# Optimization experiments

Measured on AMD Instinct MI355X. Metric: run time of the kernel, lower is better.

Reference implementation:

```python
import jax, jax.numpy as jnp
import numpy as np

N_NODES = 100000

def gcn_conv(x, row, col, w, W, b, n):
    # PyG GCNConv with edge weights: add self-loops, symmetric normalization.
    loop = jnp.arange(n)
    r = jnp.concatenate([row, loop])
    c = jnp.concatenate([col, loop])
    ew = jnp.concatenate([w, jnp.ones((n,), dtype=x.dtype)])
    deg = jax.ops.segment_sum(ew, c, num_segments=n)          # [N]
    dinv = jnp.where(deg > 0, jax.lax.rsqrt(deg), 0.0)
    norm = dinv[r] * ew * dinv[c]                              # [E+N]
    h = x @ W                                                  # [N, C]
    msg = norm[:, None] * h[r]                                 # [E+N, C]
    out = jax.ops.segment_sum(msg, c, num_segments=n)          # [N, C]
    return out + b

def setup_inputs() -> dict:
    key = jax.random.key(0)
    ks = jax.random.split(key, 9)
    n, F, H, O = N_NODES, 128, 128, 64  # H = 2*out_channels
    E = 1600000
    x = jax.random.normal(ks[0], (n, F), dtype=jnp.float32)
    edge_index = jax.random.randint(ks[1], (2, E), 0, n, dtype=jnp.int64)
    edge_attr = jax.random.uniform(ks[2], (E,), dtype=jnp.float32)
    s = 1.0 / np.sqrt(F)
    W1 = jax.random.uniform(ks[3], (F, H), jnp.float32, -s, s)
    b1 = jnp.zeros((H,), jnp.float32)
    s2 = 1.0 / np.sqrt(H)
    Wmu = jax.random.uniform(ks[4], (H, O), jnp.float32, -s2, s2)
    bmu = jnp.zeros((O,), jnp.float32)
    Wls = jax.random.uniform(ks[5], (H, O), jnp.float32, -s2, s2)
    bls = jnp.zeros((O,), jnp.float32)
    return {"x": x, "edge_index": edge_index, "edge_attr": edge_attr,
            "W1": W1, "b1": b1, "Wmu": Wmu, "bmu": bmu, "Wls": Wls, "bls": bls}

def reference(x, edge_index, edge_attr, W1, b1, Wmu, bmu, Wls, bls):
    n = x.shape[0]
    row, col = edge_index[0], edge_index[1]
    h = jax.nn.relu(gcn_conv(x, row, col, edge_attr, W1, b1, n))
    mu = gcn_conv(h, row, col, edge_attr, Wmu, bmu, n)
    logstd = gcn_conv(h, row, col, edge_attr, Wls, bls, n)
    return (mu, logstd)
```

## Files before the change

kernel.cpp:

```cpp
#include <hip/hip_runtime.h>
#include <math.h>


#define NBLK 1024

typedef __attribute__((ext_vector_type(8))) short bf16x8;
typedef __attribute__((ext_vector_type(4))) float f32x4;

__device__ __forceinline__ unsigned short f2bf_rne(float f) {
  unsigned int u = __float_as_uint(f);
  u += 0x7FFFu + ((u >> 16) & 1u);
  return (unsigned short)(u >> 16);
}

__device__ __forceinline__ float bf2f(unsigned short h) {
  return __uint_as_float(((unsigned int)h) << 16);
}

__device__ __forceinline__ unsigned int pack2(unsigned short a, unsigned short b) {
  return (unsigned int)a | ((unsigned int)b << 16);
}


__global__ __launch_bounds__(256) void hist_coarse(const int* __restrict__ col,
                                                   int* __restrict__ G,
                                                   int E, int nbuck, int epb) {
  __shared__ int h[512];
  int blk = blockIdx.x;
  for (int i = threadIdx.x; i < nbuck; i += 256) h[i] = 0;
  __syncthreads();
  int beg = blk * epb;
  int end = min(beg + epb, E);
  for (int p = beg + threadIdx.x; p < end; p += 256)
    atomicAdd(&h[col[p] >> 8], 1);
  __syncthreads();
  for (int i = threadIdx.x; i < nbuck; i += 256)
    G[(size_t)i * NBLK + blk] = h[i];
}

__global__ __launch_bounds__(1024) void scan_bucket(int* __restrict__ G,
                                                    int* __restrict__ tot) {
  __shared__ int s[NBLK];
  int b = blockIdx.x;
  int v = G[(size_t)b * NBLK + threadIdx.x];
  s[threadIdx.x] = v;
  __syncthreads();
  for (int off = 1; off < NBLK; off <<= 1) {
    int t = (threadIdx.x >= off) ? s[threadIdx.x - off] : 0;
    __syncthreads();
    s[threadIdx.x] += t;
    __syncthreads();
  }
  G[(size_t)b * NBLK + threadIdx.x] = s[threadIdx.x] - v;
  if (threadIdx.x == NBLK - 1) tot[b] = s[NBLK - 1];
}

__global__ __launch_bounds__(512) void scan_start(const int* __restrict__ tot,
                                                  int* __restrict__ start,
                                                  int* __restrict__ row_ptr,
                                                  int nbuck, int N, int E) {
  __shared__ int s[512];
  int v = (threadIdx.x < nbuck) ? tot[threadIdx.x] : 0;
  s[threadIdx.x] = v;
  __syncthreads();
  for (int off = 1; off < 512; off <<= 1) {
    int t = (threadIdx.x >= off) ? s[threadIdx.x - off] : 0;
    __syncthreads();
    s[threadIdx.x] += t;
    __syncthreads();
  }
  if (threadIdx.x < nbuck) start[threadIdx.x] = s[threadIdx.x] - v;
  if (threadIdx.x == 511) start[nbuck] = s[511];
  if (threadIdx.x == 0) row_ptr[N] = E;
}

__global__ __launch_bounds__(256) void partition_edges(
    const int* __restrict__ row, const int* __restrict__ col,
    const float* __restrict__ w, const int* __restrict__ G,
    const int* __restrict__ start, int2* __restrict__ part,
    int E, int nbuck, int epb) {
  __shared__ int cur[512];
  int blk = blockIdx.x;
  for (int i = threadIdx.x; i < nbuck; i += 256)
    cur[i] = start[i] + G[(size_t)i * NBLK + blk];
  __syncthreads();
  int beg = blk * epb;
  int end = min(beg + epb, E);
  for (int p = beg + threadIdx.x; p < end; p += 256) {
    int c = col[p];
    int pos = atomicAdd(&cur[c >> 8], 1);
    part[pos] = make_int2(row[p] | ((c & 255) << 17),
                          __float_as_int(w[p]));
  }
}

__global__ __launch_bounds__(256) void build_fine(const int* __restrict__ start,
                                                  const int2* __restrict__ part,
                                                  int* __restrict__ row_ptr,
                                                  int2* __restrict__ csr,
                                                  int N) {
  __shared__ int hist[256];
  __shared__ int sc[256];
  __shared__ int cur[256];
  int b = blockIdx.x;
  int ebeg = start[b], eend = start[b + 1];
  hist[threadIdx.x] = 0;
  __syncthreads();
  for (int p = ebeg + threadIdx.x; p < eend; p += 256)
    atomicAdd(&hist[(part[p].x >> 17) & 255], 1);
  __syncthreads();
  int v = hist[threadIdx.x];
  sc[threadIdx.x] = v;
  __syncthreads();
  for (int off = 1; off < 256; off <<= 1) {
    int t = (threadIdx.x >= off) ? sc[threadIdx.x - off] : 0;
    __syncthreads();
    sc[threadIdx.x] += t;
    __syncthreads();
  }
  int ex = sc[threadIdx.x] - v;
  int node = b * 256 + threadIdx.x;
  if (node < N) row_ptr[node] = ebeg + ex;
  cur[threadIdx.x] = ebeg + ex;
  __syncthreads();
  for (int p = ebeg + threadIdx.x; p < eend; p += 256) {
    int2 r = part[p];
    int cl = (r.x >> 17) & 255;
    int pos = atomicAdd(&cur[cl], 1);
    csr[pos] = make_int2(r.x & 0x1FFFF, r.y);
  }
}

__global__ void deg_dinv(const int* __restrict__ row_ptr, const int2* __restrict__ csr,
                         float* __restrict__ dinv, int n) {
  int i = blockIdx.x * blockDim.x + threadIdx.x;
  if (i >= n) return;
  float s = 1.0f;
  int end = row_ptr[i + 1];
  for (int p = row_ptr[i]; p < end; ++p) s += __int_as_float(csr[p].y);
  dinv[i] = 1.0f / sqrtf(s);
}

__global__ void prep_wt(const float* __restrict__ Wsrc,
                        unsigned short* __restrict__ wt_hi,
                        unsigned short* __restrict__ wt_lo) {
  int i = blockIdx.x * blockDim.x + threadIdx.x;
  if (i >= 128 * 128) return;
  int n = i & 127, k = i >> 7;
  float f = Wsrc[(size_t)k * 128 + n];
  unsigned short h = f2bf_rne(f);
  unsigned short l = f2bf_rne(f - bf2f(h));
  wt_hi[(size_t)n * 128 + k] = h;
  wt_lo[(size_t)n * 128 + k] = l;
}

__global__ void prep_wcat_t(const float* __restrict__ Wmu, const float* __restrict__ Wls,
                            const float* __restrict__ bmu, const float* __restrict__ bls,
                            unsigned short* __restrict__ wt_hi,
                            unsigned short* __restrict__ wt_lo,
                            float* __restrict__ bcat) {
  int i = blockIdx.x * blockDim.x + threadIdx.x;
  if (i >= 128 * 128) return;
  int n = i & 127, k = i >> 7;
  float f = (n < 64) ? Wmu[(size_t)k * 64 + n] : Wls[(size_t)k * 64 + (n - 64)];
  unsigned short h = f2bf_rne(f);
  unsigned short l = f2bf_rne(f - bf2f(h));
  wt_hi[(size_t)n * 128 + k] = h;
  wt_lo[(size_t)n * 128 + k] = l;
  if (i < 128) bcat[i] = (i < 64) ? bmu[i] : bls[i - 64];
}

__global__ __launch_bounds__(256) void gemm_mfma(
    const float* __restrict__ A,
    const unsigned short* __restrict__ WtHi, const unsigned short* __restrict__ WtLo,
    const float* __restrict__ bias, const float* __restrict__ rowscale,
    float* __restrict__ C0, float* __restrict__ C1,
    unsigned short* __restrict__ Cbf, int split, int M) {
  __shared__ uint4 sAhi[1024];
  __shared__ uint4 sAlo[1024];
  __shared__ uint4 sWhi[1024];
  __shared__ uint4 sWlo[1024];

  int tid = threadIdx.x;
  int lane = tid & 63, wid = tid >> 6;
  int wave_r = (wid >> 1) * 64, wave_c = (wid & 1) * 64;
  int lrow = lane & 15, lkb = lane >> 4;
  int rowBase = blockIdx.x * 128;

  f32x4 acc[4][4];
#pragma unroll
  for (int mr = 0; mr < 4; ++mr)
#pragma unroll
    for (int nc = 0; nc < 4; ++nc) acc[mr][nc] = (f32x4){0.f, 0.f, 0.f, 0.f};

  const uint4* WtHi4 = (const uint4*)WtHi;
  const uint4* WtLo4 = (const uint4*)WtLo;

  for (int kt = 0; kt < 128; kt += 64) {
    __syncthreads();
#pragma unroll
    for (int j = 0; j < 4; ++j) {
      int g = tid + 256 * j;
      int c = g >> 3, k8 = g & 7;
      int slot = k8 ^ (c & 7);
      sWhi[c * 8 + slot] = WtHi4[c * 16 + (kt >> 3) + k8];
      sWlo[c * 8 + slot] = WtLo4[c * 16 + (kt >> 3) + k8];
    }
#pragma unroll
    for (int j = 0; j < 4; ++j) {
      int g = tid + 256 * j;
      int r = g >> 3, k8 = g & 7;
      int grow = rowBase + r;
      float4 v0 = make_float4(0.f, 0.f, 0.f, 0.f);
      float4 v1 = v0;
      if (grow < M) {
        const float4* Ar = (const float4*)(A + (size_t)grow * 128 + kt);
        v0 = Ar[k8 * 2];
        v1 = Ar[k8 * 2 + 1];
      }
      float f[8] = {v0.x, v0.y, v0.z, v0.w, v1.x, v1.y, v1.z, v1.w};
      unsigned short h[8], l[8];
#pragma unroll
      for (int q = 0; q < 8; ++q) {
        h[q] = f2bf_rne(f[q]);
        l[q] = f2bf_rne(f[q] - bf2f(h[q]));
      }
      int slot = k8 ^ (r & 7);
      sAhi[r * 8 + slot] = make_uint4(pack2(h[0], h[1]), pack2(h[2], h[3]),
                                      pack2(h[4], h[5]), pack2(h[6], h[7]));
      sAlo[r * 8 + slot] = make_uint4(pack2(l[0], l[1]), pack2(l[2], l[3]),
                                      pack2(l[4], l[5]), pack2(l[6], l[7]));
    }
    __syncthreads();
#pragma unroll
    for (int ks = 0; ks < 2; ++ks) {
      bf16x8 ah[4], al[4], bh[4], bl[4];
#pragma unroll
      for (int mr = 0; mr < 4; ++mr) {
        int r = wave_r + mr * 16 + lrow;
        int slot = (ks * 4 + lkb) ^ (r & 7);
        ah[mr] = *(const bf16x8*)&sAhi[r * 8 + slot];
        al[mr] = *(const bf16x8*)&sAlo[r * 8 + slot];
      }
#pragma unroll
      for (int nc = 0; nc < 4; ++nc) {
        int c = wave_c + nc * 16 + lrow;
        int slot = (ks * 4 + lkb) ^ (c & 7);
        bh[nc] = *(const bf16x8*)&sWhi[c * 8 + slot];
        bl[nc] = *(const bf16x8*)&sWlo[c * 8 + slot];
      }
#pragma unroll
      for (int mr = 0; mr < 4; ++mr)
#pragma unroll
        for (int nc = 0; nc < 4; ++nc) {
          acc[mr][nc] = __builtin_amdgcn_mfma_f32_16x16x32_bf16(
              ah[mr], bh[nc], acc[mr][nc], 0, 0, 0);
          acc[mr][nc] = __builtin_amdgcn_mfma_f32_16x16x32_bf16(
              al[mr], bh[nc], acc[mr][nc], 0, 0, 0);
          acc[mr][nc] = __builtin_amdgcn_mfma_f32_16x16x32_bf16(
              ah[mr], bl[nc], acc[mr][nc], 0, 0, 0);
        }
    }
  }

#pragma unroll
  for (int mr = 0; mr < 4; ++mr) {
    int Rb = rowBase + wave_r + mr * 16 + lkb * 4;
    float sc[4];
#pragma unroll
    for (int reg = 0; reg < 4; ++reg)
      sc[reg] = (rowscale && (Rb + reg) < M) ? rowscale[Rb + reg] : 1.0f;
#pragma unroll
    for (int nc = 0; nc < 4; ++nc) {
      int c = wave_c + nc * 16 + lrow;
      float bb = bias ? bias[c] : 0.f;
      f32x4 v = acc[mr][nc];
#pragma unroll
      for (int reg = 0; reg < 4; ++reg) {
        int R = Rb + reg;
        if (R >= M) continue;
        float val = v[reg] * sc[reg] + bb;
        if (Cbf) Cbf[(size_t)R * 128 + c] = f2bf_rne(val);
        if (C0) {
          if (c < split) C0[(size_t)R * split + c] = val;
          else           C1[(size_t)R * split + (c - split)] = val;
        }
      }
    }
  }
}

__global__ __launch_bounds__(256) void aggregate(
    const ushort4* __restrict__ hin, const int* __restrict__ row_ptr,
    const int2* __restrict__ csr, const float* __restrict__ dinv,
    const float4* __restrict__ bias4, ushort4* __restrict__ hout_bf,
    float4* __restrict__ hout_f4, int n, int do_relu, int scale_out) {
  int node = blockIdx.x * 8 + (threadIdx.x >> 5);
  if (node >= n) return;
  int t = threadIdx.x & 31;
  int beg = row_ptr[node], end = row_ptr[node + 1];
  ushort4 hs = hin[(size_t)node * 32 + t];
  float4 acc = make_float4(bf2f(hs.x), bf2f(hs.y), bf2f(hs.z), bf2f(hs.w));
  int p = beg;
  for (; p + 4 <= end; p += 4) {
    int2 e0 = csr[p + 0];
    int2 e1 = csr[p + 1];
    int2 e2 = csr[p + 2];
    int2 e3 = csr[p + 3];
    ushort4 h0 = hin[(size_t)e0.x * 32 + t];
    ushort4 h1 = hin[(size_t)e1.x * 32 + t];
    ushort4 h2 = hin[(size_t)e2.x * 32 + t];
    ushort4 h3 = hin[(size_t)e3.x * 32 + t];
    float w0 = __int_as_float(e0.y), w1 = __int_as_float(e1.y);
    float w2 = __int_as_float(e2.y), w3 = __int_as_float(e3.y);
    acc.x = fmaf(w0, bf2f(h0.x), acc.x); acc.y = fmaf(w0, bf2f(h0.y), acc.y);
    acc.z = fmaf(w0, bf2f(h0.z), acc.z); acc.w = fmaf(w0, bf2f(h0.w), acc.w);
    acc.x = fmaf(w1, bf2f(h1.x), acc.x); acc.y = fmaf(w1, bf2f(h1.y), acc.y);
    acc.z = fmaf(w1, bf2f(h1.z), acc.z); acc.w = fmaf(w1, bf2f(h1.w), acc.w);
    acc.x = fmaf(w2, bf2f(h2.x), acc.x); acc.y = fmaf(w2, bf2f(h2.y), acc.y);
    acc.z = fmaf(w2, bf2f(h2.z), acc.z); acc.w = fmaf(w2, bf2f(h2.w), acc.w);
    acc.x = fmaf(w3, bf2f(h3.x), acc.x); acc.y = fmaf(w3, bf2f(h3.y), acc.y);
    acc.z = fmaf(w3, bf2f(h3.z), acc.z); acc.w = fmaf(w3, bf2f(h3.w), acc.w);
  }
  for (; p < end; ++p) {
    int2 e = csr[p];
    ushort4 hv = hin[(size_t)e.x * 32 + t];
    float wv = __int_as_float(e.y);
    acc.x = fmaf(wv, bf2f(hv.x), acc.x); acc.y = fmaf(wv, bf2f(hv.y), acc.y);
    acc.z = fmaf(wv, bf2f(hv.z), acc.z); acc.w = fmaf(wv, bf2f(hv.w), acc.w);
  }
  float dc = dinv[node];
  float4 val = make_float4(dc * acc.x, dc * acc.y, dc * acc.z, dc * acc.w);
  if (bias4) {
    float4 b = bias4[t];
    val.x += b.x; val.y += b.y; val.z += b.z; val.w += b.w;
  }
  if (do_relu) {
    val.x = fmaxf(val.x, 0.f); val.y = fmaxf(val.y, 0.f);
    val.z = fmaxf(val.z, 0.f); val.w = fmaxf(val.w, 0.f);
  }
  if (scale_out) {
    val.x *= dc; val.y *= dc; val.z *= dc; val.w *= dc;
  }
  size_t o = (size_t)node * 32 + t;
  if (hout_bf) {
    ushort4 ov;
    ov.x = f2bf_rne(val.x); ov.y = f2bf_rne(val.y);
    ov.z = f2bf_rne(val.z); ov.w = f2bf_rne(val.w);
    hout_bf[o] = ov;
  }
  if (hout_f4) hout_f4[o] = val;
}

extern "C" void kernel_launch(void* const* d_in, const int* in_sizes, int n_in,
                              void* d_out, int out_size, void* d_ws, size_t ws_size,
                              hipStream_t stream) {
  const float* x   = (const float*)d_in[0];
  const int*   ei  = (const int*)d_in[1];
  const float* ea  = (const float*)d_in[2];
  const float* W1  = (const float*)d_in[3];
  const float* b1  = (const float*)d_in[4];
  const float* Wmu = (const float*)d_in[5];
  const float* bmu = (const float*)d_in[6];
  const float* Wls = (const float*)d_in[7];
  const float* bls = (const float*)d_in[8];
  const int N = in_sizes[0] / 128;
  const int E = in_sizes[2];
  const int* row = ei;
  const int* col = ei + E;

  char* p = (char*)d_ws;
  auto alloc = [&](size_t bytes) -> void* {
    void* r = (void*)p;
    p += (bytes + 255) & ~(size_t)255;
    return r;
  };
  float* dinv    = (float*)alloc((size_t)N * 4);
  int*   row_ptr = (int*)alloc((size_t)(N + 1) * 4);
  unsigned short* w1t_hi = (unsigned short*)alloc(128 * 128 * 2);
  unsigned short* w1t_lo = (unsigned short*)alloc(128 * 128 * 2);
  unsigned short* wct_hi = (unsigned short*)alloc(128 * 128 * 2);
  unsigned short* wct_lo = (unsigned short*)alloc(128 * 128 * 2);
  float* bcat    = (float*)alloc(128 * 4);
  int2*  csr     = (int2*)alloc((size_t)E * 8);
  float* bufA    = (float*)alloc((size_t)N * 128 * 4);
  unsigned short* bufB = (unsigned short*)alloc((size_t)N * 128 * 2);
  unsigned short* bufC = (unsigned short*)alloc((size_t)N * 128 * 2);

  int2* part  = (int2*)bufA;
  int*  G     = (int*)bufB;
  int*  tot   = (int*)((char*)bufB + (size_t)512 * NBLK * 4);
  int*  start = tot + 512;

  float* out_mu = (float*)d_out;
  float* out_ls = out_mu + (size_t)N * 64;

  const int nbuck = (N + 255) >> 8;
  const int epb   = (E + NBLK - 1) / NBLK;
  int nbN = (N + 255) / 256;

  prep_wt<<<64, 256, 0, stream>>>(W1, w1t_hi, w1t_lo);
  prep_wcat_t<<<64, 256, 0, stream>>>(Wmu, Wls, bmu, bls, wct_hi, wct_lo, bcat);

  hist_coarse<<<NBLK, 256, 0, stream>>>(col, G, E, nbuck, epb);
  scan_bucket<<<nbuck, NBLK, 0, stream>>>(G, tot);
  scan_start<<<1, 512, 0, stream>>>(tot, start, row_ptr, nbuck, N, E);
  partition_edges<<<NBLK, 256, 0, stream>>>(row, col, ea, G, start, part,
                                            E, nbuck, epb);
  build_fine<<<nbuck, 256, 0, stream>>>(start, part, row_ptr, csr, N);
  deg_dinv<<<nbN, 256, 0, stream>>>(row_ptr, csr, dinv, N);

  int gblocks = (N + 127) / 128;
  int ablocks = (N + 7) / 8;
  gemm_mfma<<<gblocks, 256, 0, stream>>>(x, w1t_hi, w1t_lo, nullptr, dinv,
                                         nullptr, nullptr, bufB, 128, N);
  aggregate<<<ablocks, 256, 0, stream>>>((const ushort4*)bufB, row_ptr, csr, dinv,
                                         (const float4*)b1, (ushort4*)bufC,
                                         nullptr, N, 1, 1);
  aggregate<<<ablocks, 256, 0, stream>>>((const ushort4*)bufC, row_ptr, csr, dinv,
                                         nullptr, nullptr, (float4*)bufA, N, 0, 0);
  gemm_mfma<<<gblocks, 256, 0, stream>>>(bufA, wct_hi, wct_lo, bcat, nullptr,
                                         out_mu, out_ls, nullptr, 64, N);
}
```

Before: 283.6 us.

## Fuse degree computation into CSR build and deepen aggregate edge unroll

Removes the separate deg_dinv kernel by accumulating per-node weighted degree with LDS float atomics inside build_fine, writing dinv there. This saves a kernel launch and a second pass over the CSR. The aggregate kernel now batches 8 edges per iteration instead of 4, putting more gather loads in flight. The start array moves to its own workspace allocation, and its last entry is set to E directly. The extra LDS atomics and wider unroll add register and LDS pressure, and the float atomic order changes the summation order of degrees.

```diff
diff --git a/kernel.cpp b/kernel.cpp
--- a/kernel.cpp
+++ b/kernel.cpp
@@ -19,6 +19,15 @@
 
 __device__ __forceinline__ unsigned int pack2(unsigned short a, unsigned short b) {
   return (unsigned int)a | ((unsigned int)b << 16);
+}
+
+__device__ __forceinline__ void lds_fadd(float* addr, float v) {
+  unsigned int off = (unsigned int)(size_t)addr;
+  asm volatile("ds_add_f32 %0, %1" : : "v"(off), "v"(v) : "memory");
+}
+
+__device__ __forceinline__ void ds_drain() {
+  asm volatile("s_waitcnt lgkmcnt(0)" ::: "memory");
 }
 
 
@@ -70,7 +79,7 @@
     __syncthreads();
   }
   if (threadIdx.x < nbuck) start[threadIdx.x] = s[threadIdx.x] - v;
-  if (threadIdx.x == 511) start[nbuck] = s[511];
+  if (threadIdx.x == 511) start[nbuck] = E;
   if (threadIdx.x == 0) row_ptr[N] = E;
 }
 
@@ -98,16 +107,24 @@
                                                   const int2* __restrict__ part,
                                                   int* __restrict__ row_ptr,
                                                   int2* __restrict__ csr,
+                                                  float* __restrict__ dinv,
                                                   int N) {
   __shared__ int hist[256];
   __shared__ int sc[256];
   __shared__ int cur[256];
+  __shared__ float deg[256];
   int b = blockIdx.x;
   int ebeg = start[b], eend = start[b + 1];
   hist[threadIdx.x] = 0;
-  __syncthreads();
-  for (int p = ebeg + threadIdx.x; p < eend; p += 256)
-    atomicAdd(&hist[(part[p].x >> 17) & 255], 1);
+  deg[threadIdx.x] = 0.f;
+  __syncthreads();
+  for (int p = ebeg + threadIdx.x; p < eend; p += 256) {
+    int2 e = part[p];
+    int dl = (e.x >> 17) & 255;
+    atomicAdd(&hist[dl], 1);
+    lds_fadd(&deg[dl], __int_as_float(e.y));
+  }
+  ds_drain();
   __syncthreads();
   int v = hist[threadIdx.x];
   sc[threadIdx.x] = v;
@@ -120,25 +137,17 @@
   }
   int ex = sc[threadIdx.x] - v;
   int node = b * 256 + threadIdx.x;
-  if (node < N) row_ptr[node] = ebeg + ex;
+  if (node < N) {
+    row_ptr[node] = ebeg + ex;
+    dinv[node] = 1.0f / sqrtf(1.0f + deg[threadIdx.x]);
+  }
   cur[threadIdx.x] = ebeg + ex;
   __syncthreads();
   for (int p = ebeg + threadIdx.x; p < eend; p += 256) {
     int2 r = part[p];
-    int cl = (r.x >> 17) & 255;
-    int pos = atomicAdd(&cur[cl], 1);
+    int pos = atomicAdd(&cur[(r.x >> 17) & 255], 1);
     csr[pos] = make_int2(r.x & 0x1FFFF, r.y);
   }
-}
-
-__global__ void deg_dinv(const int* __restrict__ row_ptr, const int2* __restrict__ csr,
-                         float* __restrict__ dinv, int n) {
-  int i = blockIdx.x * blockDim.x + threadIdx.x;
-  if (i >= n) return;
-  float s = 1.0f;
-  int end = row_ptr[i + 1];
-  for (int p = row_ptr[i]; p < end; ++p) s += __int_as_float(csr[p].y);
-  dinv[i] = 1.0f / sqrtf(s);
 }
 
 __global__ void prep_wt(const float* __restrict__ Wsrc,
@@ -302,25 +311,21 @@
   ushort4 hs = hin[(size_t)node * 32 + t];
   float4 acc = make_float4(bf2f(hs.x), bf2f(hs.y), bf2f(hs.z), bf2f(hs.w));
   int p = beg;
-  for (; p + 4 <= end; p += 4) {
-    int2 e0 = csr[p + 0];
-    int2 e1 = csr[p + 1];
-    int2 e2 = csr[p + 2];
-    int2 e3 = csr[p + 3];
-    ushort4 h0 = hin[(size_t)e0.x * 32 + t];
-    ushort4 h1 = hin[(size_t)e1.x * 32 + t];
-    ushort4 h2 = hin[(size_t)e2.x * 32 + t];
-    ushort4 h3 = hin[(size_t)e3.x * 32 + t];
-    float w0 = __int_as_float(e0.y), w1 = __int_as_float(e1.y);
-    float w2 = __int_as_float(e2.y), w3 = __int_as_float(e3.y);
-    acc.x = fmaf(w0, bf2f(h0.x), acc.x); acc.y = fmaf(w0, bf2f(h0.y), acc.y);
-    acc.z = fmaf(w0, bf2f(h0.z), acc.z); acc.w = fmaf(w0, bf2f(h0.w), acc.w);
-    acc.x = fmaf(w1, bf2f(h1.x), acc.x); acc.y = fmaf(w1, bf2f(h1.y), acc.y);
-    acc.z = fmaf(w1, bf2f(h1.z), acc.z); acc.w = fmaf(w1, bf2f(h1.w), acc.w);
-    acc.x = fmaf(w2, bf2f(h2.x), acc.x); acc.y = fmaf(w2, bf2f(h2.y), acc.y);
-    acc.z = fmaf(w2, bf2f(h2.z), acc.z); acc.w = fmaf(w2, bf2f(h2.w), acc.w);
-    acc.x = fmaf(w3, bf2f(h3.x), acc.x); acc.y = fmaf(w3, bf2f(h3.y), acc.y);
-    acc.z = fmaf(w3, bf2f(h3.z), acc.z); acc.w = fmaf(w3, bf2f(h3.w), acc.w);
+  for (; p + 8 <= end; p += 8) {
+    int2 e[8];
+    ushort4 h[8];
+#pragma unroll
+    for (int q = 0; q < 8; ++q) e[q] = csr[p + q];
+#pragma unroll
+    for (int q = 0; q < 8; ++q) h[q] = hin[(size_t)e[q].x * 32 + t];
+#pragma unroll
+    for (int q = 0; q < 8; ++q) {
+      float wv = __int_as_float(e[q].y);
+      acc.x = fmaf(wv, bf2f(h[q].x), acc.x);
+      acc.y = fmaf(wv, bf2f(h[q].y), acc.y);
+      acc.z = fmaf(wv, bf2f(h[q].z), acc.z);
+      acc.w = fmaf(wv, bf2f(h[q].w), acc.w);
+    }
   }
   for (; p < end; ++p) {
     int2 e = csr[p];
@@ -377,6 +382,7 @@
   };
   float* dinv    = (float*)alloc((size_t)N * 4);
   int*   row_ptr = (int*)alloc((size_t)(N + 1) * 4);
+  int*   start   = (int*)alloc(520 * 4);
   unsigned short* w1t_hi = (unsigned short*)alloc(128 * 128 * 2);
   unsigned short* w1t_lo = (unsigned short*)alloc(128 * 128 * 2);
   unsigned short* wct_hi = (unsigned short*)alloc(128 * 128 * 2);
@@ -387,17 +393,15 @@
   unsigned short* bufB = (unsigned short*)alloc((size_t)N * 128 * 2);
   unsigned short* bufC = (unsigned short*)alloc((size_t)N * 128 * 2);
 
-  int2* part  = (int2*)bufA;
-  int*  G     = (int*)bufB;
-  int*  tot   = (int*)((char*)bufB + (size_t)512 * NBLK * 4);
-  int*  start = tot + 512;
+  const int nbuck = (N + 255) >> 8;
+  const int epb   = (E + NBLK - 1) / NBLK;
+
+  int2* part = (int2*)bufA;
+  int*  G    = (int*)bufB;
+  int*  tot  = (int*)((char*)bufB + (size_t)nbuck * NBLK * 4);
 
   float* out_mu = (float*)d_out;
   float* out_ls = out_mu + (size_t)N * 64;
-
-  const int nbuck = (N + 255) >> 8;
-  const int epb   = (E + NBLK - 1) / NBLK;
-  int nbN = (N + 255) / 256;
 
   prep_wt<<<64, 256, 0, stream>>>(W1, w1t_hi, w1t_lo);
   prep_wcat_t<<<64, 256, 0, stream>>>(Wmu, Wls, bmu, bls, wct_hi, wct_lo, bcat);
@@ -407,8 +411,7 @@
   scan_start<<<1, 512, 0, stream>>>(tot, start, row_ptr, nbuck, N, E);
   partition_edges<<<NBLK, 256, 0, stream>>>(row, col, ea, G, start, part,
                                             E, nbuck, epb);
-  build_fine<<<nbuck, 256, 0, stream>>>(start, part, row_ptr, csr, N);
-  deg_dinv<<<nbN, 256, 0, stream>>>(row_ptr, csr, dinv, N);
+  build_fine<<<nbuck, 256, 0, stream>>>(start, part, row_ptr, csr, dinv, N);
 
   int gblocks = (N + 127) / 128;
   int ablocks = (N + 7) / 8;
```

After: 289.5 us. +2.1%, slower.
